# Performance work log

Measured on AMD Instinct MI355X. Metric: run time of the kernel, lower is better.

The kernel has to match this reference:

```python
import jax, jax.numpy as jnp
import numpy as np

D_MODEL = 1024
N_HEADS = 16
D_HEAD = D_MODEL // N_HEADS


def setup_inputs() -> dict:
    key = jax.random.key(0)
    ks = jax.random.split(key, 7)
    x = jax.random.normal(ks[0], (1, 4096, D_MODEL), dtype=jnp.float32)
    # torch Linear default init ~ U(-1/sqrt(fan_in), 1/sqrt(fan_in)); small randn is fine for a reference
    Wqkv = jax.random.normal(ks[1], (3 * D_MODEL, D_MODEL), dtype=jnp.float32) * (1.0 / np.sqrt(D_MODEL))
    bqkv = jax.random.normal(ks[2], (3 * D_MODEL,), dtype=jnp.float32) * 0.01
    Wo = jax.random.normal(ks[3], (D_MODEL, D_MODEL), dtype=jnp.float32) * (1.0 / np.sqrt(D_MODEL))
    bo = jax.random.normal(ks[4], (D_MODEL,), dtype=jnp.float32) * 0.01
    wq = jnp.ones((D_HEAD,), dtype=jnp.float32)
    wk = jnp.ones((D_HEAD,), dtype=jnp.float32)
    return {"x": x, "Wqkv": Wqkv, "bqkv": bqkv, "Wo": Wo, "bo": bo, "wq": wq, "wk": wk}


def _rmsnorm(x, w):
    # matches RMSNormRef: mean of squares over last dim, eps added to mean before sqrt
    xf = x.astype(jnp.float32)
    rms = jnp.mean(xf * xf, axis=-1, keepdims=True)
    return (xf / jnp.sqrt(rms + 1e-6) * w.astype(jnp.float32)).astype(x.dtype)


def reference(x, Wqkv, bqkv, Wo, bo, wq, wk):
    b, s, d = x.shape
    qkv = x @ Wqkv.T + bqkv                       # [b, s, 3d]
    q, k, v = jnp.split(qkv, 3, axis=-1)
    q = q.reshape(b, s, N_HEADS, D_HEAD)
    k = k.reshape(b, s, N_HEADS, D_HEAD)
    v = v.reshape(b, s, N_HEADS, D_HEAD)
    q = _rmsnorm(q, wq)
    k = _rmsnorm(k, wk)
    # NOTE: original applies NO 1/sqrt(d_head) scaling and NO causal mask
    qf = q.astype(jnp.float32)
    kf = k.astype(jnp.float32)
    vf = v.astype(jnp.float32)
    attn = jnp.einsum('bqhd,bkhd->bhqk', qf, kf)  # [b, h, s, s] fp32 scores
    attn = jax.nn.softmax(attn, axis=-1)
    z = jnp.einsum('bhqk,bkhd->bqhd', attn, vf).astype(x.dtype)
    z = z.reshape(b, s, d)
    return z @ Wo.T + bo
```

## Files before the change

### kernel.cpp

```cpp
#include <hip/hip_runtime.h>
#include <hip/hip_bf16.h>

typedef __bf16 bf16;
typedef bf16 bf16x8 __attribute__((ext_vector_type(8)));
typedef bf16 bf16x4 __attribute__((ext_vector_type(4)));
typedef float f32x4 __attribute__((ext_vector_type(4)));
typedef float f32x16 __attribute__((ext_vector_type(16)));
typedef unsigned int u32;
typedef u32 u32x4 __attribute__((ext_vector_type(4)));

static constexpr int SEQ    = 4096;
static constexpr int DMODEL = 1024;
static constexpr int NHEADS = 16;
static constexpr int DHEAD  = 64;
static constexpr int QKV3   = 3 * DMODEL;
static constexpr float SMAX = 64.0f;
static constexpr float LOG2E = 1.44269504088896341f;

__device__ inline void gld16(const bf16* g, bf16* l) {
    __builtin_amdgcn_global_load_lds(
        (const __attribute__((address_space(1))) void*)g,
        (__attribute__((address_space(3))) void*)l, 16, 0, 0);
}

__device__ inline bf16x8 load8(const float* src) {
    float4 a = *(const float4*)(src);
    float4 b = *(const float4*)(src + 4);
    bf16x8 r;
    r[0] = (bf16)a.x; r[1] = (bf16)a.y; r[2] = (bf16)a.z; r[3] = (bf16)a.w;
    r[4] = (bf16)b.x; r[5] = (bf16)b.y; r[6] = (bf16)b.z; r[7] = (bf16)b.w;
    return r;
}

__device__ inline f32x16 zero16() {
    f32x16 r;
#pragma unroll
    for (int i = 0; i < 16; ++i) r[i] = 0.f;
    return r;
}

static constexpr size_t NX = (size_t)SEQ * DMODEL;
static constexpr size_t NW = (size_t)QKV3 * DMODEL;
static constexpr size_t NO = (size_t)DMODEL * DMODEL;

__global__ __launch_bounds__(256)
void cvt_all(const float* __restrict__ x, const float* __restrict__ Wqkv,
             const float* __restrict__ Wo, bf16* __restrict__ outbase) {
    const size_t e = ((size_t)blockIdx.x * 256 + threadIdx.x) * 8;
    const float* src;
    if (e < NX)            src = x + e;
    else if (e < NX + NW)  src = Wqkv + (e - NX);
    else                   src = Wo + (e - NX - NW);
    *(bf16x8*)(outbase + e) = load8(src);
}

__global__ __launch_bounds__(256)
void gemm_qkv(const bf16* __restrict__ A, const bf16* __restrict__ W,
              const float* __restrict__ bias, const float* __restrict__ wq,
              const float* __restrict__ wk, bf16* __restrict__ qkv,
              bf16* __restrict__ Vt) {
    __shared__ __align__(16) bf16 As[128 * 32];
    __shared__ __align__(16) bf16 Ws[128 * 32];
    const int tid  = threadIdx.x;
    const int wave = tid >> 6;
    const int ll   = tid & 15;
    const int quad = (tid & 63) >> 4;
    const int wm   = (wave >> 1) * 64;
    const int wn   = (wave & 1) * 64;
    const int m0 = blockIdx.y * 128;
    const int n0 = blockIdx.x * 128;

    f32x4 acc[4][4];
#pragma unroll
    for (int i = 0; i < 4; ++i)
#pragma unroll
        for (int j = 0; j < 4; ++j) acc[i][j] = (f32x4){0.f, 0.f, 0.f, 0.f};

    for (int k0 = 0; k0 < DMODEL; k0 += 32) {
        __syncthreads();
#pragma unroll
        for (int i = 0; i < 2; ++i) {
            const int idx = i * 256 + tid;
            const int row = idx >> 2;
            const int c   = (idx & 3) ^ ((row >> 1) & 3);
            gld16(&A[(size_t)(m0 + row) * DMODEL + k0 + c * 8], As + idx * 8);
            gld16(&W[(size_t)(n0 + row) * DMODEL + k0 + c * 8], Ws + idx * 8);
        }
        __syncthreads();
        bf16x8 af[4], bfr[4];
#pragma unroll
        for (int mi = 0; mi < 4; ++mi) {
            const int row = wm + mi * 16 + ll;
            af[mi] = *(const bf16x8*)(As + (row * 4 + (quad ^ ((ll >> 1) & 3))) * 8);
        }
#pragma unroll
        for (int ni = 0; ni < 4; ++ni) {
            const int row = wn + ni * 16 + ll;
            bfr[ni] = *(const bf16x8*)(Ws + (row * 4 + (quad ^ ((ll >> 1) & 3))) * 8);
        }
#pragma unroll
        for (int mi = 0; mi < 4; ++mi)
#pragma unroll
            for (int ni = 0; ni < 4; ++ni)
                acc[mi][ni] = __builtin_amdgcn_mfma_f32_16x16x32_bf16(
                    af[mi], bfr[ni], acc[mi][ni], 0, 0, 0);
    }

    float bvn[4];
#pragma unroll
    for (int ni = 0; ni < 4; ++ni) bvn[ni] = bias[n0 + wn + ni * 16 + ll];

    const int sect = (n0 + wn) >> 10;
    if (sect < 2) {
        const float* wv = sect ? wk : wq;
        float wvl[4];
#pragma unroll
        for (int ni = 0; ni < 4; ++ni) wvl[ni] = wv[ni * 16 + ll];
#pragma unroll
        for (int mi = 0; mi < 4; ++mi)
#pragma unroll
            for (int r = 0; r < 4; ++r) {
                float xf[4];
                float ss = 0.f;
#pragma unroll
                for (int ni = 0; ni < 4; ++ni) {
                    xf[ni] = (float)(bf16)(acc[mi][ni][r] + bvn[ni]);
                    ss += xf[ni] * xf[ni];
                }
#pragma unroll
                for (int off = 1; off < 16; off <<= 1) ss += __shfl_xor(ss, off);
                const float scale = rsqrtf(ss * (1.0f / 64.0f) + 1e-6f);
                const int row = m0 + wm + mi * 16 + quad * 4 + r;
#pragma unroll
                for (int ni = 0; ni < 4; ++ni)
                    qkv[(size_t)row * QKV3 + n0 + wn + ni * 16 + ll] =
                        (bf16)(xf[ni] * scale * wvl[ni]);
            }
    } else {
        const int h = (n0 + wn - 2 * DMODEL) >> 6;
#pragma unroll
        for (int mi = 0; mi < 4; ++mi) {
            const int kv = m0 + wm + mi * 16 + quad * 4;
#pragma unroll
            for (int ni = 0; ni < 4; ++ni) {
                bf16x4 vv;
#pragma unroll
                for (int r = 0; r < 4; ++r) vv[r] = (bf16)(acc[mi][ni][r] + bvn[ni]);
                *(bf16x4*)(Vt + (size_t)(h * DHEAD + ni * 16 + ll) * SEQ + kv) = vv;
            }
        }
    }
}

__global__ __launch_bounds__(256)
void gemm_out(const bf16* __restrict__ A, const bf16* __restrict__ W,
              const float* __restrict__ bias, float* __restrict__ C) {
    __shared__ __align__(16) bf16 As[128 * 32];
    __shared__ __align__(16) bf16 Ws[64 * 32];
    const int tid  = threadIdx.x;
    const int wave = tid >> 6;
    const int ll   = tid & 15;
    const int quad = (tid & 63) >> 4;
    const int m0 = blockIdx.y * 128;
    const int n0 = blockIdx.x * 64;

    f32x4 acc[2][4];
#pragma unroll
    for (int i = 0; i < 2; ++i)
#pragma unroll
        for (int j = 0; j < 4; ++j) acc[i][j] = (f32x4){0.f, 0.f, 0.f, 0.f};

    for (int k0 = 0; k0 < DMODEL; k0 += 32) {
        __syncthreads();
#pragma unroll
        for (int i = 0; i < 2; ++i) {
            const int idx = i * 256 + tid;
            const int row = idx >> 2;
            const int c   = (idx & 3) ^ ((row >> 1) & 3);
            gld16(&A[(size_t)(m0 + row) * DMODEL + k0 + c * 8], As + idx * 8);
        }
        {
            const int j   = tid;
            const int row = j >> 2;
            const int c   = (j & 3) ^ ((row >> 1) & 3);
            gld16(&W[(size_t)(n0 + row) * DMODEL + k0 + c * 8], Ws + j * 8);
        }
        __syncthreads();
        bf16x8 af[2], bfr[4];
#pragma unroll
        for (int mi = 0; mi < 2; ++mi) {
            const int row = wave * 32 + mi * 16 + ll;
            af[mi] = *(const bf16x8*)(As + (row * 4 + (quad ^ ((ll >> 1) & 3))) * 8);
        }
#pragma unroll
        for (int ni = 0; ni < 4; ++ni) {
            const int row = ni * 16 + ll;
            bfr[ni] = *(const bf16x8*)(Ws + (row * 4 + (quad ^ ((ll >> 1) & 3))) * 8);
        }
#pragma unroll
        for (int mi = 0; mi < 2; ++mi)
#pragma unroll
            for (int ni = 0; ni < 4; ++ni)
                acc[mi][ni] = __builtin_amdgcn_mfma_f32_16x16x32_bf16(
                    af[mi], bfr[ni], acc[mi][ni], 0, 0, 0);
    }
#pragma unroll
    for (int ni = 0; ni < 4; ++ni) {
        const int col = n0 + ni * 16 + ll;
        const float bv = bias[col];
#pragma unroll
        for (int mi = 0; mi < 2; ++mi)
#pragma unroll
            for (int r = 0; r < 4; ++r) {
                const int row = m0 + wave * 32 + mi * 16 + quad * 4 + r;
                C[(size_t)row * DMODEL + col] = acc[mi][ni][r] + bv;
            }
    }
}

template<bool PARTIAL>
__global__ __launch_bounds__(256, 2)
void attn_fwd(const bf16* __restrict__ qkv, const bf16* __restrict__ Vt,
              bf16* __restrict__ z, float* __restrict__ opf,
              float* __restrict__ lsum) {
    __shared__ __align__(16) bf16 KV[2][2][64 * 64];
    float (*Os)[32][36] = (float(*)[32][36])(&KV[0][0][0]);
    bf16* Qs = &KV[0][0][0];

    const int tid  = threadIdx.x;
    const int wave = tid >> 6;
    const int lane = tid & 63;
    const int l31  = lane & 31;
    const int hh   = lane >> 5;
    const int l7   = lane & 7;
    const int head = blockIdx.x;
    const int q0   = blockIdx.y * 256;
    const int half = PARTIAL ? blockIdx.z : 0;
    const int kvbeg = half * (SEQ / 2);
    const int kvlen = PARTIAL ? (SEQ / 2) : SEQ;
    const int nt    = kvlen / 64;

    const bf16* kbase  = qkv + DMODEL + head * DHEAD;
    const bf16* vtbase = Vt + (size_t)head * DHEAD * SEQ;

    auto stage_kv = [&](int buf, int kv0) {
#pragma unroll
        for (int i = 0; i < 2; ++i) {
            const int idx = i * 256 + tid;
            const int row = idx >> 3;
            const int c   = (idx & 7) ^ (row & 7);
            gld16(kbase + (size_t)(kv0 + row) * QKV3 + c * 8, &KV[buf][0][0] + idx * 8);
            gld16(vtbase + (size_t)row * SEQ + kv0 + c * 8, &KV[buf][1][0] + idx * 8);
        }
    };

#pragma unroll
    for (int i = 0; i < 8; ++i) {
        const int idx = i * 256 + tid;
        const int row = idx >> 3;
        const int c   = (idx & 7) ^ (row & 7);
        gld16(qkv + (size_t)(q0 + row) * QKV3 + head * DHEAD + c * 8, Qs + idx * 8);
    }
    __syncthreads();
    bf16x8 qf[4][2];
#pragma unroll
    for (int kd = 0; kd < 4; ++kd)
#pragma unroll
        for (int qs = 0; qs < 2; ++qs) {
            const int row = wave * 64 + qs * 32 + l31;
            qf[kd][qs] = *(const bf16x8*)(Qs + (row * 8 + ((kd * 2 + hh) ^ l7)) * 8);
        }
    __syncthreads();
    stage_kv(0, kvbeg);
    __syncthreads();

    f32x16 o[2][2];
    o[0][0] = zero16(); o[0][1] = zero16();
    o[1][0] = zero16(); o[1][1] = zero16();
    float lpa[2][4] = {{0.f, 0.f, 0.f, 0.f}, {0.f, 0.f, 0.f, 0.f}};

    int cur = 0;
    for (int t = 0; t < nt; ++t) {
        if (t + 1 < nt) stage_kv(cur ^ 1, kvbeg + (t + 1) * 64);
        const bf16* Ks  = &KV[cur][0][0];
        const bf16* VTs = &KV[cur][1][0];

#pragma unroll
        for (int kvt = 0; kvt < 2; ++kvt) {
            f32x16 st0 = zero16(), st1 = zero16();
            __builtin_amdgcn_s_setprio(1);
#pragma unroll
            for (int kd = 0; kd < 4; ++kd) {
                bf16x8 kf = *(const bf16x8*)(
                    Ks + ((kvt * 32 + l31) * 8 + ((kd * 2 + hh) ^ l7)) * 8);
                st0 = __builtin_amdgcn_mfma_f32_32x32x16_bf16(kf, qf[kd][0], st0, 0, 0, 0);
                st1 = __builtin_amdgcn_mfma_f32_32x32x16_bf16(kf, qf[kd][1], st1, 0, 0, 0);
            }
            __builtin_amdgcn_s_setprio(0);

            float pf0[16], pf1[16];
#pragma unroll
            for (int r = 0; r < 16; ++r)
                pf0[r] = __builtin_amdgcn_exp2f(
                    __builtin_fmaf(st0[r], LOG2E, -SMAX * LOG2E));
#pragma unroll
            for (int r = 0; r < 16; ++r)
                pf1[r] = __builtin_amdgcn_exp2f(
                    __builtin_fmaf(st1[r], LOG2E, -SMAX * LOG2E));
#pragma unroll
            for (int r = 0; r < 16; ++r) lpa[0][r & 3] += pf0[r];
#pragma unroll
            for (int r = 0; r < 16; ++r) lpa[1][r & 3] += pf1[r];

#pragma unroll
            for (int cc = 0; cc < 2; ++cc) {
                u32 a1, b1, a2, b2, a3, b3, a4, b4;
                asm("v_cvt_pk_bf16_f32 %0, %1, %2" : "=v"(a1) : "v"(pf0[8 * cc + 0]), "v"(pf0[8 * cc + 1]));
                asm("v_cvt_pk_bf16_f32 %0, %1, %2" : "=v"(b1) : "v"(pf0[8 * cc + 4]), "v"(pf0[8 * cc + 5]));
                asm("v_cvt_pk_bf16_f32 %0, %1, %2" : "=v"(a2) : "v"(pf0[8 * cc + 2]), "v"(pf0[8 * cc + 3]));
                asm("v_cvt_pk_bf16_f32 %0, %1, %2" : "=v"(b2) : "v"(pf0[8 * cc + 6]), "v"(pf0[8 * cc + 7]));
                asm("v_permlane32_swap_b32 %0, %1" : "+v"(a1), "+v"(b1));
                asm("v_permlane32_swap_b32 %0, %1" : "+v"(a2), "+v"(b2));
                asm("v_cvt_pk_bf16_f32 %0, %1, %2" : "=v"(a3) : "v"(pf1[8 * cc + 0]), "v"(pf1[8 * cc + 1]));
                asm("v_cvt_pk_bf16_f32 %0, %1, %2" : "=v"(b3) : "v"(pf1[8 * cc + 4]), "v"(pf1[8 * cc + 5]));
                asm("v_cvt_pk_bf16_f32 %0, %1, %2" : "=v"(a4) : "v"(pf1[8 * cc + 2]), "v"(pf1[8 * cc + 3]));
                asm("v_cvt_pk_bf16_f32 %0, %1, %2" : "=v"(b4) : "v"(pf1[8 * cc + 6]), "v"(pf1[8 * cc + 7]));
                asm("v_permlane32_swap_b32 %0, %1" : "+v"(a3), "+v"(b3));
                asm("v_permlane32_swap_b32 %0, %1" : "+v"(a4), "+v"(b4));
                u32x4 w0, w1;
                w0[0] = a1; w0[1] = a2; w0[2] = b1; w0[3] = b2;
                w1[0] = a3; w1[1] = a4; w1[2] = b3; w1[3] = b4;
                const bf16x8 bp0 = *(const bf16x8*)&w0;
                const bf16x8 bp1 = *(const bf16x8*)&w1;
                const int c = kvt * 2 + cc;
                __builtin_amdgcn_s_setprio(1);
#pragma unroll
                for (int dt = 0; dt < 2; ++dt) {
                    bf16x8 vf = *(const bf16x8*)(
                        VTs + ((dt * 32 + l31) * 8 + ((c * 2 + hh) ^ l7)) * 8);
                    o[dt][0] = __builtin_amdgcn_mfma_f32_32x32x16_bf16(vf, bp0, o[dt][0], 0, 0, 0);
                    o[dt][1] = __builtin_amdgcn_mfma_f32_32x32x16_bf16(vf, bp1, o[dt][1], 0, 0, 0);
                }
                __builtin_amdgcn_s_setprio(0);
            }
        }
        __syncthreads();
        cur ^= 1;
    }

#pragma unroll
    for (int qs = 0; qs < 2; ++qs) {
        float lp = (lpa[qs][0] + lpa[qs][1]) + (lpa[qs][2] + lpa[qs][3]);
        lp += __shfl_xor(lp, 32);
        const int qrow = q0 + wave * 64 + qs * 32 + l31;
        if (PARTIAL) {
            if (lane < 32) lsum[((size_t)half * SEQ + qrow) * NHEADS + head] = lp;
        }
        const float inv = PARTIAL ? 1.0f : 1.0f / lp;

#pragma unroll
        for (int dt = 0; dt < 2; ++dt) {
#pragma unroll
            for (int r = 0; r < 16; ++r) {
                const int dl = (r & 3) + 8 * (r >> 2) + 4 * hh;
                Os[wave][l31][dl] = o[dt][qs][r] * inv;
            }
#pragma unroll
            for (int it = 0; it < 4; ++it) {
                const int qr  = it * 8 + (lane >> 3);
                const int dl2 = (lane & 7) * 4;
                const f32x4 v = *(const f32x4*)(&Os[wave][qr][dl2]);
                const int row = q0 + wave * 64 + qs * 32 + qr;
                const int col = head * DHEAD + dt * 32 + dl2;
                if (PARTIAL) {
                    *(f32x4*)(opf + ((size_t)half * SEQ + row) * DMODEL + col) = v;
                } else {
                    bf16x4 ov;
                    ov[0] = (bf16)v[0]; ov[1] = (bf16)v[1];
                    ov[2] = (bf16)v[2]; ov[3] = (bf16)v[3];
                    *(bf16x4*)(z + (size_t)row * DMODEL + col) = ov;
                }
            }
        }
    }
}

__global__ __launch_bounds__(256)
void combine_halves(const float* __restrict__ opf, const float* __restrict__ lsum,
                    bf16* __restrict__ z) {
    const int row = blockIdx.x;
    const int c   = threadIdx.x * 4;
    const int head = c >> 6;
    const float l = lsum[(size_t)row * NHEADS + head] +
                    lsum[((size_t)SEQ + row) * NHEADS + head];
    const float4 o0 = *(const float4*)(opf + (size_t)row * DMODEL + c);
    const float4 o1 = *(const float4*)(opf + ((size_t)SEQ + row) * DMODEL + c);
    bf16x4 out;
    out[0] = (bf16)((o0.x + o1.x) / l);
    out[1] = (bf16)((o0.y + o1.y) / l);
    out[2] = (bf16)((o0.z + o1.z) / l);
    out[3] = (bf16)((o0.w + o1.w) / l);
    *(bf16x4*)(z + (size_t)row * DMODEL + c) = out;
}

extern "C" void kernel_launch(void* const* d_in, const int* in_sizes, int n_in,
                              void* d_out, int out_size, void* d_ws, size_t ws_size,
                              hipStream_t stream) {
    const float* x    = (const float*)d_in[0];
    const float* Wqkv = (const float*)d_in[1];
    const float* bqkv = (const float*)d_in[2];
    const float* Wo   = (const float*)d_in[3];
    const float* bo   = (const float*)d_in[4];
    const float* wq   = (const float*)d_in[5];
    const float* wk   = (const float*)d_in[6];
    float* out = (float*)d_out;

    bf16* qkv  = (bf16*)d_ws;
    bf16* z    = qkv + (size_t)SEQ * QKV3;
    bf16* Vt   = z + (size_t)SEQ * DMODEL;
    bf16* xb   = Vt + (size_t)NHEADS * DHEAD * SEQ;
    bf16* Wqb  = xb + NX;
    bf16* Wob  = Wqb + NW;
    bf16* endb = Wob + NO;
    float* opf  = (float*)endb;
    float* lsum = opf + (size_t)2 * SEQ * DMODEL;
    const size_t need = (size_t)((char*)(lsum + (size_t)2 * SEQ * NHEADS) - (char*)d_ws);
    const bool split = ws_size >= need;

    cvt_all<<<dim3((NX + NW + NO) / 2048), 256, 0, stream>>>(x, Wqkv, Wo, xb);

    gemm_qkv<<<dim3(QKV3 / 128, SEQ / 128), 256, 0, stream>>>(
        xb, Wqb, bqkv, wq, wk, qkv, Vt);

    if (split) {
        attn_fwd<true><<<dim3(NHEADS, SEQ / 256, 2), 256, 0, stream>>>(
            qkv, Vt, z, opf, lsum);
        combine_halves<<<dim3(SEQ), 256, 0, stream>>>(opf, lsum, z);
    } else {
        attn_fwd<false><<<dim3(NHEADS, SEQ / 256, 1), 256, 0, stream>>>(
            qkv, Vt, z, nullptr, nullptr);
    }

    gemm_out<<<dim3(DMODEL / 64, SEQ / 128), 256, 0, stream>>>(z, Wob, bo, out);
}
```

Measured before the change: 234.7 us.

## Split KV range across waves within block, drop separate combine kernel

Each attention block now handles 64 queries of one head, and its four waves each process a quarter of the KV sequence in their own LDS double buffer. Tiles are staged through registers without block-wide barriers, and the partial outputs are reduced in shared memory at the end. This removes the fp32 partial-output round trip through global memory, the combine_halves launch and the per-tile __syncthreads. In exchange each wave loads its own K/V so K/V traffic per query grows, and a blockIdx swizzle is added for cache locality.

```diff
diff --git a/kernel.cpp b/kernel.cpp
--- a/kernel.cpp
+++ b/kernel.cpp
@@ -218,14 +218,13 @@
     }
 }
 
-template<bool PARTIAL>
 __global__ __launch_bounds__(256, 2)
 void attn_fwd(const bf16* __restrict__ qkv, const bf16* __restrict__ Vt,
-              bf16* __restrict__ z, float* __restrict__ opf,
-              float* __restrict__ lsum) {
-    __shared__ __align__(16) bf16 KV[2][2][64 * 64];
-    float (*Os)[32][36] = (float(*)[32][36])(&KV[0][0][0]);
-    bf16* Qs = &KV[0][0][0];
+              bf16* __restrict__ z) {
+    __shared__ __align__(16) bf16 QS[64 * 64];
+    __shared__ __align__(16) bf16 KVW[4][2][4096];
+    float* Os4 = (float*)&KVW[0][0][0];
+    float* l4  = (float*)&QS[0];
 
     const int tid  = threadIdx.x;
     const int wave = tid >> 6;
@@ -233,33 +232,22 @@
     const int l31  = lane & 31;
     const int hh   = lane >> 5;
     const int l7   = lane & 7;
-    const int head = blockIdx.x;
-    const int q0   = blockIdx.y * 256;
-    const int half = PARTIAL ? blockIdx.z : 0;
-    const int kvbeg = half * (SEQ / 2);
-    const int kvlen = PARTIAL ? (SEQ / 2) : SEQ;
-    const int nt    = kvlen / 64;
+
+    const int nid  = (blockIdx.x & 7) * 128 + (blockIdx.x >> 3);
+    const int head = nid >> 6;
+    const int q0   = (nid & 63) * 64;
 
     const bf16* kbase  = qkv + DMODEL + head * DHEAD;
     const bf16* vtbase = Vt + (size_t)head * DHEAD * SEQ;
-
-    auto stage_kv = [&](int buf, int kv0) {
-#pragma unroll
-        for (int i = 0; i < 2; ++i) {
-            const int idx = i * 256 + tid;
-            const int row = idx >> 3;
-            const int c   = (idx & 7) ^ (row & 7);
-            gld16(kbase + (size_t)(kv0 + row) * QKV3 + c * 8, &KV[buf][0][0] + idx * 8);
-            gld16(vtbase + (size_t)row * SEQ + kv0 + c * 8, &KV[buf][1][0] + idx * 8);
-        }
-    };
-
-#pragma unroll
-    for (int i = 0; i < 8; ++i) {
+    const int kvw0 = wave * (SEQ / 4);
+    constexpr int NT = (SEQ / 4) / 32;
+
+#pragma unroll
+    for (int i = 0; i < 2; ++i) {
         const int idx = i * 256 + tid;
         const int row = idx >> 3;
         const int c   = (idx & 7) ^ (row & 7);
-        gld16(qkv + (size_t)(q0 + row) * QKV3 + head * DHEAD + c * 8, Qs + idx * 8);
+        gld16(qkv + (size_t)(q0 + row) * QKV3 + head * DHEAD + c * 8, QS + idx * 8);
     }
     __syncthreads();
     bf16x8 qf[4][2];
@@ -267,140 +255,145 @@
     for (int kd = 0; kd < 4; ++kd)
 #pragma unroll
         for (int qs = 0; qs < 2; ++qs) {
-            const int row = wave * 64 + qs * 32 + l31;
-            qf[kd][qs] = *(const bf16x8*)(Qs + (row * 8 + ((kd * 2 + hh) ^ l7)) * 8);
-        }
-    __syncthreads();
-    stage_kv(0, kvbeg);
-    __syncthreads();
+            const int row = qs * 32 + l31;
+            qf[kd][qs] = *(const bf16x8*)(QS + (row * 8 + ((kd * 2 + hh) ^ l7)) * 8);
+        }
+
+    bf16* const myKV = &KVW[wave][0][0];
+
+    u32x4 kr[4], vr[4];
+    auto issue_loads = [&](int kv0) {
+#pragma unroll
+        for (int j = 0; j < 4; ++j) {
+            const int idx = j * 64 + lane;
+            {
+                const int row = idx >> 3, c = (idx & 7) ^ (row & 7);
+                kr[j] = *(const u32x4*)(kbase + (size_t)(kv0 + row) * QKV3 + c * 8);
+            }
+            {
+                const int row = idx >> 2, c = (idx & 3) ^ (row & 3);
+                vr[j] = *(const u32x4*)(vtbase + (size_t)row * SEQ + kv0 + c * 8);
+            }
+        }
+    };
+    auto write_tile = [&](int buf) {
+        bf16* Kd = myKV + buf * 4096;
+#pragma unroll
+        for (int j = 0; j < 4; ++j) {
+            const int idx = j * 64 + lane;
+            *(u32x4*)(Kd + idx * 8)        = kr[j];
+            *(u32x4*)(Kd + 2048 + idx * 8) = vr[j];
+        }
+    };
+
+    issue_loads(kvw0);
+    write_tile(0);
 
     f32x16 o[2][2];
     o[0][0] = zero16(); o[0][1] = zero16();
     o[1][0] = zero16(); o[1][1] = zero16();
     float lpa[2][4] = {{0.f, 0.f, 0.f, 0.f}, {0.f, 0.f, 0.f, 0.f}};
 
-    int cur = 0;
-    for (int t = 0; t < nt; ++t) {
-        if (t + 1 < nt) stage_kv(cur ^ 1, kvbeg + (t + 1) * 64);
-        const bf16* Ks  = &KV[cur][0][0];
-        const bf16* VTs = &KV[cur][1][0];
-
-#pragma unroll
-        for (int kvt = 0; kvt < 2; ++kvt) {
-            f32x16 st0 = zero16(), st1 = zero16();
+#pragma unroll 1
+    for (int t = 0; t < NT; ++t) {
+        if (t + 1 < NT) issue_loads(kvw0 + (t + 1) * 32);
+        const bf16* Kd = myKV + (t & 1) * 4096;
+        const bf16* Vd = Kd + 2048;
+
+        f32x16 st0 = zero16(), st1 = zero16();
+        __builtin_amdgcn_s_setprio(1);
+#pragma unroll
+        for (int kd = 0; kd < 4; ++kd) {
+            bf16x8 kf = *(const bf16x8*)(Kd + (l31 * 8 + ((kd * 2 + hh) ^ l7)) * 8);
+            st0 = __builtin_amdgcn_mfma_f32_32x32x16_bf16(kf, qf[kd][0], st0, 0, 0, 0);
+            st1 = __builtin_amdgcn_mfma_f32_32x32x16_bf16(kf, qf[kd][1], st1, 0, 0, 0);
+        }
+        __builtin_amdgcn_s_setprio(0);
+
+        float pf0[16], pf1[16];
+#pragma unroll
+        for (int r = 0; r < 16; ++r)
+            pf0[r] = __builtin_amdgcn_exp2f(__builtin_fmaf(st0[r], LOG2E, -SMAX * LOG2E));
+#pragma unroll
+        for (int r = 0; r < 16; ++r)
+            pf1[r] = __builtin_amdgcn_exp2f(__builtin_fmaf(st1[r], LOG2E, -SMAX * LOG2E));
+#pragma unroll
+        for (int r = 0; r < 16; ++r) lpa[0][r & 3] += pf0[r];
+#pragma unroll
+        for (int r = 0; r < 16; ++r) lpa[1][r & 3] += pf1[r];
+
+#pragma unroll
+        for (int cc = 0; cc < 2; ++cc) {
+            u32 a1, b1, a2, b2, a3, b3, a4, b4;
+            asm("v_cvt_pk_bf16_f32 %0, %1, %2" : "=v"(a1) : "v"(pf0[8 * cc + 0]), "v"(pf0[8 * cc + 1]));
+            asm("v_cvt_pk_bf16_f32 %0, %1, %2" : "=v"(b1) : "v"(pf0[8 * cc + 4]), "v"(pf0[8 * cc + 5]));
+            asm("v_cvt_pk_bf16_f32 %0, %1, %2" : "=v"(a2) : "v"(pf0[8 * cc + 2]), "v"(pf0[8 * cc + 3]));
+            asm("v_cvt_pk_bf16_f32 %0, %1, %2" : "=v"(b2) : "v"(pf0[8 * cc + 6]), "v"(pf0[8 * cc + 7]));
+            asm("v_permlane32_swap_b32 %0, %1" : "+v"(a1), "+v"(b1));
+            asm("v_permlane32_swap_b32 %0, %1" : "+v"(a2), "+v"(b2));
+            asm("v_cvt_pk_bf16_f32 %0, %1, %2" : "=v"(a3) : "v"(pf1[8 * cc + 0]), "v"(pf1[8 * cc + 1]));
+            asm("v_cvt_pk_bf16_f32 %0, %1, %2" : "=v"(b3) : "v"(pf1[8 * cc + 4]), "v"(pf1[8 * cc + 5]));
+            asm("v_cvt_pk_bf16_f32 %0, %1, %2" : "=v"(a4) : "v"(pf1[8 * cc + 2]), "v"(pf1[8 * cc + 3]));
+            asm("v_cvt_pk_bf16_f32 %0, %1, %2" : "=v"(b4) : "v"(pf1[8 * cc + 6]), "v"(pf1[8 * cc + 7]));
+            asm("v_permlane32_swap_b32 %0, %1" : "+v"(a3), "+v"(b3));
+            asm("v_permlane32_swap_b32 %0, %1" : "+v"(a4), "+v"(b4));
+            u32x4 w0, w1;
+            w0[0] = a1; w0[1] = a2; w0[2] = b1; w0[3] = b2;
+            w1[0] = a3; w1[1] = a4; w1[2] = b3; w1[3] = b4;
+            const bf16x8 bp0 = *(const bf16x8*)&w0;
+            const bf16x8 bp1 = *(const bf16x8*)&w1;
             __builtin_amdgcn_s_setprio(1);
 #pragma unroll
-            for (int kd = 0; kd < 4; ++kd) {
-                bf16x8 kf = *(const bf16x8*)(
-                    Ks + ((kvt * 32 + l31) * 8 + ((kd * 2 + hh) ^ l7)) * 8);
-                st0 = __builtin_amdgcn_mfma_f32_32x32x16_bf16(kf, qf[kd][0], st0, 0, 0, 0);
-                st1 = __builtin_amdgcn_mfma_f32_32x32x16_bf16(kf, qf[kd][1], st1, 0, 0, 0);
+            for (int dt = 0; dt < 2; ++dt) {
+                bf16x8 vf = *(const bf16x8*)(
+                    Vd + ((dt * 32 + l31) * 4 + ((cc * 2 + hh) ^ (l31 & 3))) * 8);
+                o[dt][0] = __builtin_amdgcn_mfma_f32_32x32x16_bf16(vf, bp0, o[dt][0], 0, 0, 0);
+                o[dt][1] = __builtin_amdgcn_mfma_f32_32x32x16_bf16(vf, bp1, o[dt][1], 0, 0, 0);
             }
             __builtin_amdgcn_s_setprio(0);
-
-            float pf0[16], pf1[16];
-#pragma unroll
-            for (int r = 0; r < 16; ++r)
-                pf0[r] = __builtin_amdgcn_exp2f(
-                    __builtin_fmaf(st0[r], LOG2E, -SMAX * LOG2E));
-#pragma unroll
-            for (int r = 0; r < 16; ++r)
-                pf1[r] = __builtin_amdgcn_exp2f(
-                    __builtin_fmaf(st1[r], LOG2E, -SMAX * LOG2E));
-#pragma unroll
-            for (int r = 0; r < 16; ++r) lpa[0][r & 3] += pf0[r];
-#pragma unroll
-            for (int r = 0; r < 16; ++r) lpa[1][r & 3] += pf1[r];
-
-#pragma unroll
-            for (int cc = 0; cc < 2; ++cc) {
-                u32 a1, b1, a2, b2, a3, b3, a4, b4;
-                asm("v_cvt_pk_bf16_f32 %0, %1, %2" : "=v"(a1) : "v"(pf0[8 * cc + 0]), "v"(pf0[8 * cc + 1]));
-                asm("v_cvt_pk_bf16_f32 %0, %1, %2" : "=v"(b1) : "v"(pf0[8 * cc + 4]), "v"(pf0[8 * cc + 5]));
-                asm("v_cvt_pk_bf16_f32 %0, %1, %2" : "=v"(a2) : "v"(pf0[8 * cc + 2]), "v"(pf0[8 * cc + 3]));
-                asm("v_cvt_pk_bf16_f32 %0, %1, %2" : "=v"(b2) : "v"(pf0[8 * cc + 6]), "v"(pf0[8 * cc + 7]));
-                asm("v_permlane32_swap_b32 %0, %1" : "+v"(a1), "+v"(b1));
-                asm("v_permlane32_swap_b32 %0, %1" : "+v"(a2), "+v"(b2));
-                asm("v_cvt_pk_bf16_f32 %0, %1, %2" : "=v"(a3) : "v"(pf1[8 * cc + 0]), "v"(pf1[8 * cc + 1]));
-                asm("v_cvt_pk_bf16_f32 %0, %1, %2" : "=v"(b3) : "v"(pf1[8 * cc + 4]), "v"(pf1[8 * cc + 5]));
-                asm("v_cvt_pk_bf16_f32 %0, %1, %2" : "=v"(a4) : "v"(pf1[8 * cc + 2]), "v"(pf1[8 * cc + 3]));
-                asm("v_cvt_pk_bf16_f32 %0, %1, %2" : "=v"(b4) : "v"(pf1[8 * cc + 6]), "v"(pf1[8 * cc + 7]));
-                asm("v_permlane32_swap_b32 %0, %1" : "+v"(a3), "+v"(b3));
-                asm("v_permlane32_swap_b32 %0, %1" : "+v"(a4), "+v"(b4));
-                u32x4 w0, w1;
-                w0[0] = a1; w0[1] = a2; w0[2] = b1; w0[3] = b2;
-                w1[0] = a3; w1[1] = a4; w1[2] = b3; w1[3] = b4;
-                const bf16x8 bp0 = *(const bf16x8*)&w0;
-                const bf16x8 bp1 = *(const bf16x8*)&w1;
-                const int c = kvt * 2 + cc;
-                __builtin_amdgcn_s_setprio(1);
-#pragma unroll
-                for (int dt = 0; dt < 2; ++dt) {
-                    bf16x8 vf = *(const bf16x8*)(
-                        VTs + ((dt * 32 + l31) * 8 + ((c * 2 + hh) ^ l7)) * 8);
-                    o[dt][0] = __builtin_amdgcn_mfma_f32_32x32x16_bf16(vf, bp0, o[dt][0], 0, 0, 0);
-                    o[dt][1] = __builtin_amdgcn_mfma_f32_32x32x16_bf16(vf, bp1, o[dt][1], 0, 0, 0);
-                }
-                __builtin_amdgcn_s_setprio(0);
-            }
-        }
-        __syncthreads();
-        cur ^= 1;
-    }
-
+        }
+
+        if (t + 1 < NT) write_tile((t + 1) & 1);
+    }
+
+    float lp[2];
 #pragma unroll
     for (int qs = 0; qs < 2; ++qs) {
-        float lp = (lpa[qs][0] + lpa[qs][1]) + (lpa[qs][2] + lpa[qs][3]);
-        lp += __shfl_xor(lp, 32);
-        const int qrow = q0 + wave * 64 + qs * 32 + l31;
-        if (PARTIAL) {
-            if (lane < 32) lsum[((size_t)half * SEQ + qrow) * NHEADS + head] = lp;
-        }
-        const float inv = PARTIAL ? 1.0f : 1.0f / lp;
-
-#pragma unroll
-        for (int dt = 0; dt < 2; ++dt) {
+        lp[qs] = (lpa[qs][0] + lpa[qs][1]) + (lpa[qs][2] + lpa[qs][3]);
+        lp[qs] += __shfl_xor(lp[qs], 32);
+    }
+#pragma unroll
+    for (int dt = 0; dt < 2; ++dt)
+#pragma unroll
+        for (int qs = 0; qs < 2; ++qs)
 #pragma unroll
             for (int r = 0; r < 16; ++r) {
                 const int dl = (r & 3) + 8 * (r >> 2) + 4 * hh;
-                Os[wave][l31][dl] = o[dt][qs][r] * inv;
-            }
-#pragma unroll
-            for (int it = 0; it < 4; ++it) {
-                const int qr  = it * 8 + (lane >> 3);
-                const int dl2 = (lane & 7) * 4;
-                const f32x4 v = *(const f32x4*)(&Os[wave][qr][dl2]);
-                const int row = q0 + wave * 64 + qs * 32 + qr;
-                const int col = head * DHEAD + dt * 32 + dl2;
-                if (PARTIAL) {
-                    *(f32x4*)(opf + ((size_t)half * SEQ + row) * DMODEL + col) = v;
-                } else {
-                    bf16x4 ov;
-                    ov[0] = (bf16)v[0]; ov[1] = (bf16)v[1];
-                    ov[2] = (bf16)v[2]; ov[3] = (bf16)v[3];
-                    *(bf16x4*)(z + (size_t)row * DMODEL + col) = ov;
-                }
-            }
-        }
-    }
-}
-
-__global__ __launch_bounds__(256)
-void combine_halves(const float* __restrict__ opf, const float* __restrict__ lsum,
-                    bf16* __restrict__ z) {
-    const int row = blockIdx.x;
-    const int c   = threadIdx.x * 4;
-    const int head = c >> 6;
-    const float l = lsum[(size_t)row * NHEADS + head] +
-                    lsum[((size_t)SEQ + row) * NHEADS + head];
-    const float4 o0 = *(const float4*)(opf + (size_t)row * DMODEL + c);
-    const float4 o1 = *(const float4*)(opf + ((size_t)SEQ + row) * DMODEL + c);
-    bf16x4 out;
-    out[0] = (bf16)((o0.x + o1.x) / l);
-    out[1] = (bf16)((o0.y + o1.y) / l);
-    out[2] = (bf16)((o0.z + o1.z) / l);
-    out[3] = (bf16)((o0.w + o1.w) / l);
-    *(bf16x4*)(z + (size_t)row * DMODEL + c) = out;
+                Os4[wave * 4096 + ((dt * 2 + qs) * 32 + dl) * 32 + l31] = o[dt][qs][r];
+            }
+    if (lane < 32) {
+        l4[(wave * 2 + 0) * 32 + l31] = lp[0];
+        l4[(wave * 2 + 1) * 32 + l31] = lp[1];
+    }
+    __syncthreads();
+
+    const int q    = tid >> 2;
+    const int dblk = (tid & 3) * 16;
+    const int qs   = q >> 5, lq = q & 31;
+    const float ltot = (l4[(0 * 2 + qs) * 32 + lq] + l4[(1 * 2 + qs) * 32 + lq]) +
+                       (l4[(2 * 2 + qs) * 32 + lq] + l4[(3 * 2 + qs) * 32 + lq]);
+    const float invl = 1.0f / ltot;
+    bf16 obuf[16];
+#pragma unroll
+    for (int k = 0; k < 16; ++k) {
+        const int d = dblk + k, dt = d >> 5, dl = d & 31;
+        const int off = ((dt * 2 + qs) * 32 + dl) * 32 + lq;
+        const float s = (Os4[off] + Os4[4096 + off]) + (Os4[8192 + off] + Os4[12288 + off]);
+        obuf[k] = (bf16)(s * invl);
+    }
+    bf16* zp = z + (size_t)(q0 + q) * DMODEL + head * DHEAD + dblk;
+    *(bf16x8*)(zp)     = *(bf16x8*)&obuf[0];
+    *(bf16x8*)(zp + 8) = *(bf16x8*)&obuf[8];
 }
 
 extern "C" void kernel_launch(void* const* d_in, const int* in_sizes, int n_in,
@@ -421,25 +414,13 @@
     bf16* xb   = Vt + (size_t)NHEADS * DHEAD * SEQ;
     bf16* Wqb  = xb + NX;
     bf16* Wob  = Wqb + NW;
-    bf16* endb = Wob + NO;
-    float* opf  = (float*)endb;
-    float* lsum = opf + (size_t)2 * SEQ * DMODEL;
-    const size_t need = (size_t)((char*)(lsum + (size_t)2 * SEQ * NHEADS) - (char*)d_ws);
-    const bool split = ws_size >= need;
 
     cvt_all<<<dim3((NX + NW + NO) / 2048), 256, 0, stream>>>(x, Wqkv, Wo, xb);
 
     gemm_qkv<<<dim3(QKV3 / 128, SEQ / 128), 256, 0, stream>>>(
         xb, Wqb, bqkv, wq, wk, qkv, Vt);
 
-    if (split) {
-        attn_fwd<true><<<dim3(NHEADS, SEQ / 256, 2), 256, 0, stream>>>(
-            qkv, Vt, z, opf, lsum);
-        combine_halves<<<dim3(SEQ), 256, 0, stream>>>(opf, lsum, z);
-    } else {
-        attn_fwd<false><<<dim3(NHEADS, SEQ / 256, 1), 256, 0, stream>>>(
-            qkv, Vt, z, nullptr, nullptr);
-    }
+    attn_fwd<<<dim3(NHEADS * (SEQ / 64)), 256, 0, stream>>>(qkv, Vt, z);
 
     gemm_out<<<dim3(DMODEL / 64, SEQ / 128), 256, 0, stream>>>(z, Wob, bo, out);
 }
```

New measurement: 249.4 us. 1.06x slower.
